# Performance work log

Measured on AMD Instinct MI355X. Metric: run time of the kernel, lower is better.

The kernel has to match this reference:

```python
import jax, jax.numpy as jnp
import numpy as np

B = 16384  # batch
D = 64     # input_size (number of causal nodes)
H = 64     # hidden_size of each per-node MLP


def setup_inputs() -> dict:
    key = jax.random.key(0)
    k1, k2, k3 = jax.random.split(key, 3)
    inputs = jax.random.normal(k1, (B, D), dtype=jnp.float32)
    adjacency = jnp.ones((D, D), dtype=jnp.float32)  # buffer initialized to ones
    # stacked per-node weights: net_i = Linear(D->H, no bias) -> ReLU -> Linear(H->1, no bias)
    W1 = jax.random.normal(k2, (D, H, D), dtype=jnp.float32) * (1.0 / np.sqrt(D))
    W2 = jax.random.normal(k3, (D, H), dtype=jnp.float32) * (1.0 / np.sqrt(H))
    return {"inputs": inputs, "adjacency": adjacency, "W1": W1, "W2": W2}


def reference(inputs, adjacency, W1, W2):
    # inputs: [B, D]; adjacency: [D, D]; W1: [D, H, D]; W2: [D, H]
    # Original: repeat inputs to [B, D, D], mask rows by adjacency, then for each
    # node i apply its tiny MLP to row i and concat the scalar outputs -> [B, D].
    masked = inputs[:, None, :] * adjacency[None, :, :]          # [B, D, D]
    h = jax.nn.relu(jnp.einsum('bid,ihd->bih', masked, W1))      # [B, D, H]
    out = jnp.einsum('bih,ih->bi', h, W2)                        # [B, D]
    return out
```

## Files before the change

### kernel.cpp

```cpp
#include <hip/hip_runtime.h>
#include <hip/hip_bf16.h>

constexpr int BN = 16384;
constexpr int DN = 64;
constexpr int HN = 64;
constexpr int W1ELEMS = DN * HN * DN;
constexpr int WCH = W1ELEMS / 4;

typedef __attribute__((ext_vector_type(8))) short short8;
typedef __attribute__((ext_vector_type(4))) float f32x4;
typedef __attribute__((ext_vector_type(2))) float f32x2;

__device__ __forceinline__ unsigned short f2bf(float f) {
    __hip_bfloat16 h = __float2bfloat16(f);
    return *reinterpret_cast<unsigned short*>(&h);
}

__device__ __forceinline__ short8 cvt8(float4 a, float4 b) {
    short8 r;
    r[0] = (short)f2bf(a.x); r[1] = (short)f2bf(a.y);
    r[2] = (short)f2bf(a.z); r[3] = (short)f2bf(a.w);
    r[4] = (short)f2bf(b.x); r[5] = (short)f2bf(b.y);
    r[6] = (short)f2bf(b.z); r[7] = (short)f2bf(b.w);
    return r;
}

#define DPP_ROR_ADD(x, N)                                                     \
    x += __int_as_float(__builtin_amdgcn_update_dpp(                          \
            0, __float_as_int(x), 0x120 + (N), 0xf, 0xf, false))

__global__ __launch_bounds__(256) void w1prep_kernel(
    const float* __restrict__ W1, const float* __restrict__ adj,
    unsigned short* __restrict__ W1bf)
{
    int c = blockIdx.x * 256 + threadIdx.x;
    int flat = c * 4;
    int i = flat >> 12;
    int d = flat & 63;
    float4 w = reinterpret_cast<const float4*>(W1)[c];
    float4 a = *reinterpret_cast<const float4*>(adj + i * DN + d);
    ushort4 o;
    o.x = f2bf(w.x * a.x); o.y = f2bf(w.y * a.y);
    o.z = f2bf(w.z * a.z); o.w = f2bf(w.w * a.w);
    reinterpret_cast<ushort4*>(W1bf)[c] = o;
}

__global__ __launch_bounds__(256, 3) void mlp_kernel(
    const float* __restrict__ X,
    const unsigned short* __restrict__ W1bf,
    const float* __restrict__ W2,
    float* __restrict__ out)
{
    const int btile = blockIdx.x & 127;
    const int ng    = blockIdx.x >> 7;
    const int wave  = threadIdx.x >> 6;
    const int lane  = threadIdx.x & 63;
    const int row16 = lane & 15;
    const int quad  = lane >> 4;

    __shared__ unsigned short ldsW1[4 * HN * DN];
    __shared__ float ldsW2[4 * HN];
    __shared__ float lds_out[128][4];

    const int b0 = btile * 128 + wave * 32;
    const float* aBase = X + (size_t)(b0 + row16) * DN + quad * 8;
    short8 afrag[2][2];
#pragma unroll
    for (int mt = 0; mt < 2; ++mt)
#pragma unroll
        for (int kk = 0; kk < 2; ++kk) {
            const float* p = aBase + mt * 16 * DN + kk * 32;
            float4 v0 = *reinterpret_cast<const float4*>(p);
            float4 v1 = *reinterpret_cast<const float4*>(p + 4);
            afrag[mt][kk] = cvt8(v0, v1);
        }

    {
        const unsigned short* gsrc = W1bf + (size_t)ng * (4 * HN * DN);
#pragma unroll
        for (int it = 0; it < 8; ++it) {
            int chunk = it * 256 + threadIdx.x;
            int nl = chunk >> 9;
            int rem = chunk & 511;
            int h = rem >> 3;
            int c = rem & 7;
            short8 v = *reinterpret_cast<const short8*>(gsrc + chunk * 8);
            int elem = nl * 4096 + h * 64 + ((c ^ (h & 7)) << 3);
            *reinterpret_cast<short8*>(&ldsW1[elem]) = v;
        }
        ldsW2[threadIdx.x] = W2[ng * 256 + threadIdx.x];
    }
    __syncthreads();

#pragma unroll
    for (int j = 0; j < 4; ++j) {
        short8 bfrag[2][4];
#pragma unroll
        for (int kk = 0; kk < 2; ++kk)
#pragma unroll
            for (int nt = 0; nt < 4; ++nt) {
                int h = nt * 16 + row16;
                int elem = j * 4096 + h * 64 + (((kk * 4 + quad) ^ (row16 & 7)) << 3);
                bfrag[kk][nt] = *reinterpret_cast<const short8*>(&ldsW1[elem]);
            }

        float w2v[4];
#pragma unroll
        for (int nt = 0; nt < 4; ++nt)
            w2v[nt] = ldsW2[j * 64 + nt * 16 + row16];

        f32x4 acc[2][4];
#pragma unroll
        for (int mt = 0; mt < 2; ++mt)
#pragma unroll
            for (int nt = 0; nt < 4; ++nt)
                acc[mt][nt] = (f32x4){0.f, 0.f, 0.f, 0.f};

#pragma unroll
        for (int kk = 0; kk < 2; ++kk)
#pragma unroll
            for (int nt = 0; nt < 4; ++nt) {
                acc[0][nt] = __builtin_amdgcn_mfma_f32_16x16x32_bf16(afrag[0][kk], bfrag[kk][nt], acc[0][nt], 0, 0, 0);
                acc[1][nt] = __builtin_amdgcn_mfma_f32_16x16x32_bf16(afrag[1][kk], bfrag[kk][nt], acc[1][nt], 0, 0, 0);
            }

#pragma unroll
        for (int mt = 0; mt < 2; ++mt) {
            f32x2 s01 = (f32x2){0.f, 0.f}, s23 = (f32x2){0.f, 0.f};
#pragma unroll
            for (int nt = 0; nt < 4; ++nt) {
                f32x2 m01 = (f32x2){fmaxf(acc[mt][nt][0], 0.f), fmaxf(acc[mt][nt][1], 0.f)};
                f32x2 m23 = (f32x2){fmaxf(acc[mt][nt][2], 0.f), fmaxf(acc[mt][nt][3], 0.f)};
                s01 += m01 * w2v[nt];
                s23 += m23 * w2v[nt];
            }
            float p[4] = {s01[0], s01[1], s23[0], s23[1]};
#pragma unroll
            for (int r = 0; r < 4; ++r) {
                DPP_ROR_ADD(p[r], 8);
                DPP_ROR_ADD(p[r], 4);
                DPP_ROR_ADD(p[r], 2);
                DPP_ROR_ADD(p[r], 1);
            }
            if (row16 < 4)
                lds_out[wave * 32 + mt * 16 + quad * 4 + row16][j] = p[row16];
        }
    }

    __syncthreads();
    if (threadIdx.x < 128) {
        int row = threadIdx.x;
        float4 v = *reinterpret_cast<const float4*>(&lds_out[row][0]);
        *reinterpret_cast<float4*>(out + (size_t)(btile * 128 + row) * DN + ng * 4) = v;
    }
}

extern "C" void kernel_launch(void* const* d_in, const int* in_sizes, int n_in,
                              void* d_out, int out_size, void* d_ws, size_t ws_size,
                              hipStream_t stream) {
    const float* X   = (const float*)d_in[0];
    const float* adj = (const float*)d_in[1];
    const float* W1  = (const float*)d_in[2];
    const float* W2  = (const float*)d_in[3];
    float* out = (float*)d_out;

    unsigned short* W1bf = (unsigned short*)d_ws;

    w1prep_kernel<<<WCH / 256, 256, 0, stream>>>(W1, adj, W1bf);
    mlp_kernel<<<128 * 16, 256, 0, stream>>>(X, W1bf, W2, out);
}
```

Before: 78.72 us.

## Fuse W1 masking/conversion into MLP kernel and transpose MFMA operand roles

Removes the separate W1 prep kernel: each block now loads fp32 W1 and adjacency, multiplies and converts them to bf16 directly into LDS. The MFMA is transposed so W1 supplies the A operand (hidden along M) and X supplies B, which lets the W2 reduction use a float4 per lane and a two-step cross-quad shuffle instead of DPP reductions plus an LDS output staging buffer and extra barrier. This saves one kernel launch and a global round trip for W1bf. In exchange, every block rereads fp32 W1 (twice the bytes) and redoes the conversion, with 128 blocks sharing each node group.

Measured after the change: 77.49 us. No clear change (-1.6%).

```diff
diff --git a/kernel.cpp b/kernel.cpp
--- a/kernel.cpp
+++ b/kernel.cpp
@@ -4,8 +4,6 @@
 constexpr int BN = 16384;
 constexpr int DN = 64;
 constexpr int HN = 64;
-constexpr int W1ELEMS = DN * HN * DN;
-constexpr int WCH = W1ELEMS / 4;
 
 typedef __attribute__((ext_vector_type(8))) short short8;
 typedef __attribute__((ext_vector_type(4))) float f32x4;
@@ -25,133 +23,114 @@
     return r;
 }
 
-#define DPP_ROR_ADD(x, N)                                                     \
-    x += __int_as_float(__builtin_amdgcn_update_dpp(                          \
-            0, __float_as_int(x), 0x120 + (N), 0xf, 0xf, false))
-
-__global__ __launch_bounds__(256) void w1prep_kernel(
-    const float* __restrict__ W1, const float* __restrict__ adj,
-    unsigned short* __restrict__ W1bf)
-{
-    int c = blockIdx.x * 256 + threadIdx.x;
-    int flat = c * 4;
-    int i = flat >> 12;
-    int d = flat & 63;
-    float4 w = reinterpret_cast<const float4*>(W1)[c];
-    float4 a = *reinterpret_cast<const float4*>(adj + i * DN + d);
-    ushort4 o;
-    o.x = f2bf(w.x * a.x); o.y = f2bf(w.y * a.y);
-    o.z = f2bf(w.z * a.z); o.w = f2bf(w.w * a.w);
-    reinterpret_cast<ushort4*>(W1bf)[c] = o;
-}
-
-__global__ __launch_bounds__(256, 3) void mlp_kernel(
+__global__ __launch_bounds__(256, 3) void mlp_fused_kernel(
     const float* __restrict__ X,
-    const unsigned short* __restrict__ W1bf,
+    const float* __restrict__ adj,
+    const float* __restrict__ W1,
     const float* __restrict__ W2,
     float* __restrict__ out)
 {
     const int btile = blockIdx.x & 127;
     const int ng    = blockIdx.x >> 7;
-    const int wave  = threadIdx.x >> 6;
-    const int lane  = threadIdx.x & 63;
+    const int tid   = threadIdx.x;
+    const int wave  = tid >> 6;
+    const int lane  = tid & 63;
     const int row16 = lane & 15;
     const int quad  = lane >> 4;
 
     __shared__ unsigned short ldsW1[4 * HN * DN];
     __shared__ float ldsW2[4 * HN];
-    __shared__ float lds_out[128][4];
 
     const int b0 = btile * 128 + wave * 32;
-    const float* aBase = X + (size_t)(b0 + row16) * DN + quad * 8;
-    short8 afrag[2][2];
+    short8 xfrag[2][2];
 #pragma unroll
-    for (int mt = 0; mt < 2; ++mt)
+    for (int kk = 0; kk < 2; ++kk)
 #pragma unroll
-        for (int kk = 0; kk < 2; ++kk) {
-            const float* p = aBase + mt * 16 * DN + kk * 32;
+        for (int nt = 0; nt < 2; ++nt) {
+            const float* p = X + (size_t)(b0 + nt * 16 + row16) * DN + kk * 32 + quad * 8;
             float4 v0 = *reinterpret_cast<const float4*>(p);
             float4 v1 = *reinterpret_cast<const float4*>(p + 4);
-            afrag[mt][kk] = cvt8(v0, v1);
+            xfrag[kk][nt] = cvt8(v0, v1);
         }
 
     {
-        const unsigned short* gsrc = W1bf + (size_t)ng * (4 * HN * DN);
+        const float4* w4 = reinterpret_cast<const float4*>(W1 + (size_t)ng * 4 * HN * DN);
+        const float4* a4 = reinterpret_cast<const float4*>(adj + (size_t)ng * 4 * DN);
 #pragma unroll
         for (int it = 0; it < 8; ++it) {
-            int chunk = it * 256 + threadIdx.x;
+            int chunk = it * 256 + tid;
             int nl = chunk >> 9;
-            int rem = chunk & 511;
-            int h = rem >> 3;
-            int c = rem & 7;
-            short8 v = *reinterpret_cast<const short8*>(gsrc + chunk * 8);
+            int h  = (chunk >> 3) & 63;
+            int c  = chunk & 7;
+            float4 w0 = w4[chunk * 2];
+            float4 w1v = w4[chunk * 2 + 1];
+            float4 a0 = a4[nl * 16 + c * 2];
+            float4 a1 = a4[nl * 16 + c * 2 + 1];
+            float4 m0 = {w0.x * a0.x, w0.y * a0.y, w0.z * a0.z, w0.w * a0.w};
+            float4 m1 = {w1v.x * a1.x, w1v.y * a1.y, w1v.z * a1.z, w1v.w * a1.w};
             int elem = nl * 4096 + h * 64 + ((c ^ (h & 7)) << 3);
-            *reinterpret_cast<short8*>(&ldsW1[elem]) = v;
+            *reinterpret_cast<short8*>(&ldsW1[elem]) = cvt8(m0, m1);
         }
-        ldsW2[threadIdx.x] = W2[ng * 256 + threadIdx.x];
+        ldsW2[tid] = W2[ng * 256 + tid];
     }
     __syncthreads();
 
+    float res[2][4];
+
 #pragma unroll
     for (int j = 0; j < 4; ++j) {
-        short8 bfrag[2][4];
+        short8 wfrag[2][4];
 #pragma unroll
         for (int kk = 0; kk < 2; ++kk)
 #pragma unroll
-            for (int nt = 0; nt < 4; ++nt) {
-                int h = nt * 16 + row16;
+            for (int mt = 0; mt < 4; ++mt) {
+                int h = mt * 16 + row16;
                 int elem = j * 4096 + h * 64 + (((kk * 4 + quad) ^ (row16 & 7)) << 3);
-                bfrag[kk][nt] = *reinterpret_cast<const short8*>(&ldsW1[elem]);
+                wfrag[kk][mt] = *reinterpret_cast<const short8*>(&ldsW1[elem]);
             }
 
-        float w2v[4];
+        float4 w2v[4];
 #pragma unroll
-        for (int nt = 0; nt < 4; ++nt)
-            w2v[nt] = ldsW2[j * 64 + nt * 16 + row16];
+        for (int mt = 0; mt < 4; ++mt)
+            w2v[mt] = *reinterpret_cast<const float4*>(&ldsW2[j * 64 + mt * 16 + quad * 4]);
 
-        f32x4 acc[2][4];
+        f32x4 acc[4][2];
 #pragma unroll
-        for (int mt = 0; mt < 2; ++mt)
+        for (int mt = 0; mt < 4; ++mt)
 #pragma unroll
-            for (int nt = 0; nt < 4; ++nt)
+            for (int nt = 0; nt < 2; ++nt)
                 acc[mt][nt] = (f32x4){0.f, 0.f, 0.f, 0.f};
 
 #pragma unroll
         for (int kk = 0; kk < 2; ++kk)
 #pragma unroll
-            for (int nt = 0; nt < 4; ++nt) {
-                acc[0][nt] = __builtin_amdgcn_mfma_f32_16x16x32_bf16(afrag[0][kk], bfrag[kk][nt], acc[0][nt], 0, 0, 0);
-                acc[1][nt] = __builtin_amdgcn_mfma_f32_16x16x32_bf16(afrag[1][kk], bfrag[kk][nt], acc[1][nt], 0, 0, 0);
+            for (int mt = 0; mt < 4; ++mt) {
+                acc[mt][0] = __builtin_amdgcn_mfma_f32_16x16x32_bf16(wfrag[kk][mt], xfrag[kk][0], acc[mt][0], 0, 0, 0);
+                acc[mt][1] = __builtin_amdgcn_mfma_f32_16x16x32_bf16(wfrag[kk][mt], xfrag[kk][1], acc[mt][1], 0, 0, 0);
             }
 
 #pragma unroll
-        for (int mt = 0; mt < 2; ++mt) {
-            f32x2 s01 = (f32x2){0.f, 0.f}, s23 = (f32x2){0.f, 0.f};
+        for (int nt = 0; nt < 2; ++nt) {
+            f32x2 s = (f32x2){0.f, 0.f};
 #pragma unroll
-            for (int nt = 0; nt < 4; ++nt) {
+            for (int mt = 0; mt < 4; ++mt) {
                 f32x2 m01 = (f32x2){fmaxf(acc[mt][nt][0], 0.f), fmaxf(acc[mt][nt][1], 0.f)};
                 f32x2 m23 = (f32x2){fmaxf(acc[mt][nt][2], 0.f), fmaxf(acc[mt][nt][3], 0.f)};
-                s01 += m01 * w2v[nt];
-                s23 += m23 * w2v[nt];
+                s += m01 * (f32x2){w2v[mt].x, w2v[mt].y};
+                s += m23 * (f32x2){w2v[mt].z, w2v[mt].w};
             }
-            float p[4] = {s01[0], s01[1], s23[0], s23[1]};
-#pragma unroll
-            for (int r = 0; r < 4; ++r) {
-                DPP_ROR_ADD(p[r], 8);
-                DPP_ROR_ADD(p[r], 4);
-                DPP_ROR_ADD(p[r], 2);
-                DPP_ROR_ADD(p[r], 1);
-            }
-            if (row16 < 4)
-                lds_out[wave * 32 + mt * 16 + quad * 4 + row16][j] = p[row16];
+            float r = s[0] + s[1];
+            r += __shfl_xor(r, 16);
+            r += __shfl_xor(r, 32);
+            res[nt][j] = r;
         }
     }
 
-    __syncthreads();
-    if (threadIdx.x < 128) {
-        int row = threadIdx.x;
-        float4 v = *reinterpret_cast<const float4*>(&lds_out[row][0]);
-        *reinterpret_cast<float4*>(out + (size_t)(btile * 128 + row) * DN + ng * 4) = v;
+    if (quad < 2) {
+        float4 v = (quad == 0)
+            ? make_float4(res[0][0], res[0][1], res[0][2], res[0][3])
+            : make_float4(res[1][0], res[1][1], res[1][2], res[1][3]);
+        *reinterpret_cast<float4*>(out + (size_t)(b0 + quad * 16 + row16) * DN + ng * 4) = v;
     }
 }
 
@@ -164,8 +143,7 @@
     const float* W2  = (const float*)d_in[3];
     float* out = (float*)d_out;
 
-    unsigned short* W1bf = (unsigned short*)d_ws;
+    (void)d_ws; (void)ws_size;
 
-    w1prep_kernel<<<WCH / 256, 256, 0, stream>>>(W1, adj, W1bf);
-    mlp_kernel<<<128 * 16, 256, 0, stream>>>(X, W1bf, W2, out);
+    mlp_fused_kernel<<<128 * 16, 256, 0, stream>>>(X, adj, W1, W2, out);
 }
```
